# Kernel tuning notes

Hardware: AMD Instinct MI355X
Metric: run time of the kernel (lower is better)

Reference implementation:

```python
import jax, jax.numpy as jnp
import numpy as np

GRID = 16
K = 2
NW = (GRID - K + 1) ** 2  # 225 sliding 2x2 windows on the 16x16 grid


def _make_mask():
    idx = np.arange(GRID * GRID).reshape(GRID, GRID)
    wins = np.stack([idx[i:i + K, j:j + K].ravel()
                     for i in range(GRID - K + 1) for j in range(GRID - K + 1)])
    m = np.zeros((NW, GRID * GRID), np.float32)
    m[np.arange(NW)[:, None], wins] = 1.0
    return jnp.asarray(m)

MASK = _make_mask()          # [225, 256] window -> covered cells
MASK_COUNT = MASK.sum(0)     # windows covering each cell
BN_SCALE = np.float32(1.0 / np.sqrt(1.0 + 1e-5))  # eval BN, running mean=0 var=1


def _adapter(x, w1, w2):
    return jax.nn.relu(jax.nn.relu(x @ w1.T) @ w2.T)


def _bn(x, g, b):
    return x * (g * BN_SCALE) + b


def _head(x, w1, b1, g2, be2, w2, b2, g3, be3, w3, b3):
    x = _bn(jax.nn.relu(x @ w1.T + b1), g2, be2)
    x = _bn(jax.nn.relu(x @ w2.T + b2), g3, be3)
    return jax.nn.sigmoid(x @ w3.T + b3)[:, 0]


def setup_inputs() -> dict:
    B, L, P, D, R, S = 64, 3, 225, 640, 1800, 240
    key = jax.random.key(0)
    ks = jax.random.split(key, 16)
    n = lambda k, s, sc=1.0: jax.random.normal(k, s, jnp.float32) * sc
    te = n(ks[3], (2, D)); te = te / jnp.linalg.norm(te, axis=-1, keepdims=True)
    pr = n(ks[5], (L, R, D)); pr = pr / jnp.linalg.norm(pr, axis=-1, keepdims=True)
    w = 0.05
    return dict(
        image=n(ks[0], (B, 3, S, S)),
        image_embeds=n(ks[1], (B, D)),
        patch_embeds=n(ks[2], (L, B, P, D)),
        text_embeds=te,
        image_embeds_ref=n(ks[4], (1, D)),
        patch_embeds_ref=pr,
        a_w1=n(ks[6], (160, D), w), a_w2=n(ks[7], (D, 160), w),
        r_w1=n(ks[8], (128, D), w), r_b1=jnp.zeros((128,)),
        r_g2=jnp.ones((128,)), r_be2=jnp.zeros((128,)),
        r_w2=n(ks[9], (64, 128), w), r_b2=jnp.zeros((64,)),
        r_g3=jnp.ones((64,)), r_be3=jnp.zeros((64,)),
        r_w3=n(ks[10], (1, 64), w), r_b3=jnp.zeros((1,)),
        h_w1=n(ks[11], (128, P), w), h_b1=jnp.zeros((128,)),
        h_g2=jnp.ones((128,)), h_be2=jnp.zeros((128,)),
        h_w2=n(ks[12], (64, 128), w), h_b2=jnp.zeros((64,)),
        h_g3=jnp.ones((64,)), h_be3=jnp.zeros((64,)),
        h_w3=n(ks[13], (1, 64), w), h_b3=jnp.zeros((1,)),
    )


def reference(image, image_embeds, patch_embeds, text_embeds, image_embeds_ref,
              patch_embeds_ref, a_w1, a_w2,
              r_w1, r_b1, r_g2, r_be2, r_w2, r_b2, r_g3, r_be3, r_w3, r_b3,
              h_w1, h_b1, h_g2, h_be2, h_w2, h_b2, h_g3, h_be3, h_w3, h_b3):
    pe = patch_embeds / jnp.linalg.norm(patch_embeds, axis=-1, keepdims=True)
    nie = image_embeds / jnp.linalg.norm(image_embeds, axis=-1, keepdims=True)
    text_score = jax.nn.softmax(100.0 * nie @ text_embeds.T, axis=-1)[:, 1]
    # kNN-style min-distance over reference patches: [L,B,P,R]
    sim = jnp.einsum('lbpd,lrd->lbpr', pe, patch_embeds_ref)
    patch_ref_map = ((1.0 - sim).min(axis=3) / 2.0).mean(axis=0)  # [B,P]
    fg_score = patch_ref_map.max(axis=1)
    diff = image_embeds_ref - _adapter(image_embeds, a_w1, a_w2)
    img_ref_score = _head(diff, r_w1, r_b1, r_g2, r_be2, r_w2, r_b2, r_g3, r_be3, r_w3, r_b3)
    holistic = (text_score + img_ref_score)[:, None] + patch_ref_map  # [B,225]
    hl_score = _head(holistic, h_w1, h_b1, h_g2, h_be2, h_w2, h_b2, h_g3, h_be3, h_w3, h_b3)
    final_score = (hl_score + fg_score) / 2.0
    # harmonic aggregation of window scores onto the 16x16 grid
    heat = (MASK_COUNT / ((1.0 / holistic) @ MASK)).reshape(-1, GRID, GRID)
    hmap = jax.image.resize(heat, (heat.shape[0], image.shape[2], image.shape[3]), 'bilinear')
    return final_score, hmap
```

## Files before the change

### kernel.cpp

```cpp
#include <hip/hip_runtime.h>
#include <stdint.h>
#include <math.h>

#define L_DIM 3
#define B_DIM 64
#define P_DIM 225
#define D_DIM 640
#define R_DIM 1800
#define S_DIM 240
#define M_TOT 14400
#define M_PAD 14592
#define N_PAD 2048
#define MT 57
#define NT 8
#define KT 10
#define BNSCALE 0.99999500003749981f

typedef __bf16 bf16x8 __attribute__((ext_vector_type(8)));
typedef float f32x4 __attribute__((ext_vector_type(4)));

__device__ __forceinline__ unsigned short f2bf(float f) {
    union { float f; unsigned u; } v; v.f = f;
    unsigned u = v.u;
    unsigned r = (u + 0x7FFFu + ((u >> 16) & 1u)) >> 16;
    return (unsigned short)r;
}

__global__ __launch_bounds__(256)
void k_convert(const float* __restrict__ pe, const float* __restrict__ per,
               unsigned short* __restrict__ abf, unsigned short* __restrict__ rbf,
               float* __restrict__ rnorm)
{
    const int AROWS = L_DIM * M_PAD;
    int wid = (blockIdx.x * 256 + threadIdx.x) >> 6;
    int lane = threadIdx.x & 63;
    const ushort4 z4 = {0, 0, 0, 0};
    if (wid < AROWS) {
        int l = wid / M_PAD, r = wid - l * M_PAD;
        unsigned short* dst = abf + (size_t)wid * D_DIM;
        if (r < M_TOT) {
            const float4* src = (const float4*)(pe + ((size_t)l * M_TOT + r) * D_DIM);
            float ss = 0.f;
            #pragma unroll
            for (int it = 0; it < 3; ++it) {
                int idx = it * 64 + lane;
                if (idx < 160) {
                    float4 v = src[idx];
                    ss += v.x * v.x + v.y * v.y + v.z * v.z + v.w * v.w;
                    ushort4 o;
                    o.x = f2bf(v.x); o.y = f2bf(v.y); o.z = f2bf(v.z); o.w = f2bf(v.w);
                    *(ushort4*)(dst + idx * 4) = o;
                }
            }
            #pragma unroll
            for (int m = 32; m; m >>= 1) ss += __shfl_xor(ss, m);
            if (lane == 0) rnorm[l * M_TOT + r] = rsqrtf(ss);
        } else {
            #pragma unroll
            for (int it = 0; it < 3; ++it) {
                int idx = it * 64 + lane;
                if (idx < 160) *(ushort4*)(dst + idx * 4) = z4;
            }
        }
    } else {
        int w2 = wid - AROWS;
        int l = w2 / N_PAD, r = w2 - l * N_PAD;
        unsigned short* dst = rbf + (size_t)w2 * D_DIM;
        if (r < R_DIM) {
            const float4* src = (const float4*)(per + ((size_t)l * R_DIM + r) * D_DIM);
            #pragma unroll
            for (int it = 0; it < 3; ++it) {
                int idx = it * 64 + lane;
                if (idx < 160) {
                    float4 v = src[idx];
                    ushort4 o;
                    o.x = f2bf(v.x); o.y = f2bf(v.y); o.z = f2bf(v.z); o.w = f2bf(v.w);
                    *(ushort4*)(dst + idx * 4) = o;
                }
            }
        } else {
            #pragma unroll
            for (int it = 0; it < 3; ++it) {
                int idx = it * 64 + lane;
                if (idx < 160) *(ushort4*)(dst + idx * 4) = z4;
            }
        }
    }
}

#define MFMA(A, B, C) __builtin_amdgcn_mfma_f32_16x16x32_bf16((A), (B), (C), 0, 0, 0)
#define GLL(SRC, DSTOFF)                                                     \
    __builtin_amdgcn_global_load_lds(                                        \
        (const __attribute__((address_space(1))) void*)(SRC),               \
        (__attribute__((address_space(3))) void*)(lds + (DSTOFF)), 16, 0, 0)

#define PHASE_TAIL(NJB, STG0, STG1, VMSTR)                                   \
    {                                                                        \
        bf16x8 b00 = *(const bf16x8*)(lds + bB + (brow0 + (NJB) * 16) * 64 + sw0);     \
        bf16x8 b01 = *(const bf16x8*)(lds + bB + (brow0 + (NJB) * 16) * 64 + sw1);     \
        bf16x8 b10 = *(const bf16x8*)(lds + bB + (brow0 + (NJB + 1) * 16) * 64 + sw0); \
        bf16x8 b11 = *(const bf16x8*)(lds + bB + (brow0 + (NJB + 1) * 16) * 64 + sw1); \
        STG0; STG1;                                                          \
        asm volatile("s_waitcnt " VMSTR ::: "memory");                       \
        __builtin_amdgcn_s_barrier();                                        \
        __builtin_amdgcn_s_setprio(1);                                       \
        _Pragma("unroll")                                                    \
        for (int mi = 0; mi < 4; ++mi) {                                     \
            acc[mi][NJB]     = MFMA(a[mi][0], b00, acc[mi][NJB]);            \
            acc[mi][NJB]     = MFMA(a[mi][1], b01, acc[mi][NJB]);            \
            acc[mi][NJB + 1] = MFMA(a[mi][0], b10, acc[mi][NJB + 1]);        \
            acc[mi][NJB + 1] = MFMA(a[mi][1], b11, acc[mi][NJB + 1]);        \
        }                                                                    \
        __builtin_amdgcn_s_setprio(0);                                       \
    }

__global__ __launch_bounds__(512, 2)
void k_gemm_max(const unsigned short* __restrict__ abf,
                const unsigned short* __restrict__ rbf,
                float* __restrict__ pmax)
{
    __shared__ unsigned short lds[65536];
    __shared__ float red[2][256];

    int bid = blockIdx.x;
    int v = (bid & 7) * 171 + (bid >> 3);
    int l = v / (MT * NT);
    int rem = v - l * (MT * NT);
    int mt = rem >> 3;
    int nt = rem & 7;

    int tid = threadIdx.x;
    int wid = tid >> 6, lane = tid & 63;
    int wm = wid >> 1;
    int wn = wid & 1;
    int lane15 = lane & 15, lg = lane >> 4;
    int sA = lane15 & 7;
    int sw0 = ((lg) ^ sA) << 3;
    int sw1 = ((4 + lg) ^ sA) << 3;
    int arow0 = wm * 64 + lane15;
    int brow0 = wn * 128 + lane15;

    int rowc = lane >> 3;
    int scol = ((lane & 7) ^ rowc) << 3;
    const unsigned short* gA = abf + (size_t)(l * M_PAD + mt * 256) * D_DIM;
    const unsigned short* gB = rbf + (size_t)(l * N_PAD + nt * 256) * D_DIM;
    int chA0 = wid, chA1 = 8 + wid, chA2 = 16 + wid, chA3 = 24 + wid;
    int chB0 = (wid < 4) ? (0 + wid) : (12 + wid);
    int chB1 = (wid < 4) ? (4 + wid) : (16 + wid);
    int chB2 = (wid < 4) ? (8 + wid) : (20 + wid);
    int chB3 = (wid < 4) ? (12 + wid) : (24 + wid);
    const unsigned short* pA0 = gA + (size_t)(chA0 * 8 + rowc) * D_DIM + scol;
    const unsigned short* pA1 = gA + (size_t)(chA1 * 8 + rowc) * D_DIM + scol;
    const unsigned short* pA2 = gA + (size_t)(chA2 * 8 + rowc) * D_DIM + scol;
    const unsigned short* pA3 = gA + (size_t)(chA3 * 8 + rowc) * D_DIM + scol;
    const unsigned short* pB0 = gB + (size_t)(chB0 * 8 + rowc) * D_DIM + scol;
    const unsigned short* pB1 = gB + (size_t)(chB1 * 8 + rowc) * D_DIM + scol;
    const unsigned short* pB2 = gB + (size_t)(chB2 * 8 + rowc) * D_DIM + scol;
    const unsigned short* pB3 = gB + (size_t)(chB3 * 8 + rowc) * D_DIM + scol;

    f32x4 acc[4][8];
    #pragma unroll
    for (int mi = 0; mi < 4; ++mi)
        #pragma unroll
        for (int nj = 0; nj < 8; ++nj)
            acc[mi][nj] = f32x4{0.f, 0.f, 0.f, 0.f};

    GLL(pA0, chA0 * 512); GLL(pA1, chA1 * 512);
    GLL(pA2, chA2 * 512); GLL(pA3, chA3 * 512);
    GLL(pB0, 32768 + chB0 * 512); GLL(pB1, 32768 + chB1 * 512);
    GLL(pB2, 32768 + chB2 * 512); GLL(pB3, 32768 + chB3 * 512);
    asm volatile("s_waitcnt vmcnt(3)" ::: "memory");
    __builtin_amdgcn_s_barrier();

    int buf = 0;
    for (int kt = 0; kt < KT; ++kt) {
        int ob = buf ^ 1;
        int aB = buf * 16384;
        int bB = 32768 + buf * 16384;
        int oaB = ob * 16384;
        int obB = 32768 + ob * 16384;
        int koff = (kt + 1 < KT ? kt + 1 : KT - 1) * 64;

        bf16x8 a[4][2];
        #pragma unroll
        for (int mi = 0; mi < 4; ++mi) {
            a[mi][0] = *(const bf16x8*)(lds + aB + (arow0 + mi * 16) * 64 + sw0);
            a[mi][1] = *(const bf16x8*)(lds + aB + (arow0 + mi * 16) * 64 + sw1);
        }
        PHASE_TAIL(0, GLL(pA0 + koff, oaB + chA0 * 512),
                      GLL(pA1 + koff, oaB + chA1 * 512), "vmcnt(4)")
        PHASE_TAIL(2, GLL(pA2 + koff, oaB + chA2 * 512),
                      GLL(pA3 + koff, oaB + chA3 * 512), "vmcnt(5)")
        PHASE_TAIL(4, GLL(pB0 + koff, obB + chB0 * 512),
                      GLL(pB1 + koff, obB + chB1 * 512), "vmcnt(6)")
        PHASE_TAIL(6, GLL(pB2 + koff, obB + chB2 * 512),
                      GLL(pB3 + koff, obB + chB3 * 512), "vmcnt(3)")
        buf = ob;
    }

    __syncthreads();

    int colbase = nt * 256 + wn * 128 + lane15;
    #pragma unroll
    for (int mi = 0; mi < 4; ++mi) {
        float t[4] = {-__builtin_inff(), -__builtin_inff(),
                      -__builtin_inff(), -__builtin_inff()};
        #pragma unroll
        for (int nj = 0; nj < 8; ++nj) {
            if (colbase + nj * 16 < R_DIM) {
                #pragma unroll
                for (int r = 0; r < 4; ++r) t[r] = fmaxf(t[r], acc[mi][nj][r]);
            }
        }
        #pragma unroll
        for (int m = 1; m <= 8; m <<= 1) {
            #pragma unroll
            for (int r = 0; r < 4; ++r) t[r] = fmaxf(t[r], __shfl_xor(t[r], m));
        }
        if (lane15 == 0) {
            int rb = wm * 64 + mi * 16 + lg * 4;
            #pragma unroll
            for (int r = 0; r < 4; ++r) red[wn][rb + r] = t[r];
        }
    }
    __syncthreads();
    if (tid < 256) {
        float vmx = fmaxf(red[0][tid], red[1][tid]);
        pmax[((size_t)l * NT + nt) * M_PAD + mt * 256 + tid] = vmx;
    }
}

__device__ __forceinline__ float block_sum8(float v, volatile float* scratch) {
    #pragma unroll
    for (int m = 32; m; m >>= 1) v += __shfl_xor(v, m);
    int w = threadIdx.x >> 6;
    __syncthreads();
    if ((threadIdx.x & 63) == 0) scratch[w] = v;
    __syncthreads();
    float r = 0.f;
    #pragma unroll
    for (int i = 0; i < 8; ++i) r += scratch[i];
    return r;
}
__device__ __forceinline__ float block_max8(float v, volatile float* scratch) {
    #pragma unroll
    for (int m = 32; m; m >>= 1) v = fmaxf(v, __shfl_xor(v, m));
    int w = threadIdx.x >> 6;
    __syncthreads();
    if ((threadIdx.x & 63) == 0) scratch[w] = v;
    __syncthreads();
    float r = scratch[0];
    #pragma unroll
    for (int i = 1; i < 8; ++i) r = fmaxf(r, scratch[i]);
    return r;
}

__global__ __launch_bounds__(512)
void k_small(const float* __restrict__ ie, const float* __restrict__ te,
             const float* __restrict__ ier,
             const float* __restrict__ a_w1, const float* __restrict__ a_w2,
             const float* __restrict__ r_w1, const float* __restrict__ r_b1,
             const float* __restrict__ r_g2, const float* __restrict__ r_be2,
             const float* __restrict__ r_w2, const float* __restrict__ r_b2,
             const float* __restrict__ r_g3, const float* __restrict__ r_be3,
             const float* __restrict__ r_w3, const float* __restrict__ r_b3,
             const float* __restrict__ h_w1, const float* __restrict__ h_b1,
             const float* __restrict__ h_g2, const float* __restrict__ h_be2,
             const float* __restrict__ h_w2, const float* __restrict__ h_b2,
             const float* __restrict__ h_g3, const float* __restrict__ h_be3,
             const float* __restrict__ h_w3, const float* __restrict__ h_b3,
             const float* __restrict__ pmax, const float* __restrict__ rnorm,
             float* __restrict__ heat, float* __restrict__ out_score)
{
    int b = blockIdx.x, tid = threadIdx.x;
    __shared__ float x[D_DIM];
    __shared__ float h1[160];
    __shared__ float dif[D_DIM];
    __shared__ float z1[128];
    __shared__ float z2[64];
    __shared__ float hol[P_DIM];
    __shared__ float rcp[P_DIM];
    __shared__ float scratch[8];

    for (int i = tid; i < D_DIM; i += 512) x[i] = ie[b * D_DIM + i];
    __syncthreads();

    float ss = 0.f, d0 = 0.f, d1 = 0.f;
    for (int i = tid; i < D_DIM; i += 512) {
        float v = x[i];
        ss += v * v;
        d0 += v * te[i];
        d1 += v * te[D_DIM + i];
    }
    float ssum = block_sum8(ss, scratch);
    float dd0 = block_sum8(d0, scratch);
    float dd1 = block_sum8(d1, scratch);
    float tscore = 1.f / (1.f + expf(100.f * rsqrtf(ssum) * (dd0 - dd1)));

    for (int o = tid; o < 160; o += 512) {
        const float* w = a_w1 + (size_t)o * D_DIM;
        float s0 = 0, s1 = 0, s2 = 0, s3 = 0;
        for (int d = 0; d < D_DIM; d += 4) {
            s0 += x[d] * w[d]; s1 += x[d + 1] * w[d + 1];
            s2 += x[d + 2] * w[d + 2]; s3 += x[d + 3] * w[d + 3];
        }
        h1[o] = fmaxf((s0 + s1) + (s2 + s3), 0.f);
    }
    __syncthreads();
    for (int d = tid; d < D_DIM; d += 512) {
        const float* w = a_w2 + (size_t)d * 160;
        float s0 = 0, s1 = 0, s2 = 0, s3 = 0;
        for (int o = 0; o < 160; o += 4) {
            s0 += h1[o] * w[o]; s1 += h1[o + 1] * w[o + 1];
            s2 += h1[o + 2] * w[o + 2]; s3 += h1[o + 3] * w[o + 3];
        }
        dif[d] = ier[d] - fmaxf((s0 + s1) + (s2 + s3), 0.f);
    }
    __syncthreads();

    for (int o = tid; o < 128; o += 512) {
        const float* w = r_w1 + (size_t)o * D_DIM;
        float s0 = 0, s1 = 0, s2 = 0, s3 = 0;
        for (int d = 0; d < D_DIM; d += 4) {
            s0 += dif[d] * w[d]; s1 += dif[d + 1] * w[d + 1];
            s2 += dif[d + 2] * w[d + 2]; s3 += dif[d + 3] * w[d + 3];
        }
        float s = (s0 + s1) + (s2 + s3) + r_b1[o];
        z1[o] = fmaxf(s, 0.f) * (r_g2[o] * BNSCALE) + r_be2[o];
    }
    __syncthreads();
    for (int o = tid; o < 64; o += 512) {
        const float* w = r_w2 + (size_t)o * 128;
        float s = r_b2[o];
        for (int d = 0; d < 128; ++d) s += z1[d] * w[d];
        z2[o] = fmaxf(s, 0.f) * (r_g3[o] * BNSCALE) + r_be3[o];
    }
    __syncthreads();
    float sp = (tid < 64) ? z2[tid] * r_w3[tid] : 0.f;
    float irs = 1.f / (1.f + expf(-(block_sum8(sp, scratch) + r_b3[0])));

    float fgp = -__builtin_inff();
    float base = tscore + irs;
    for (int p = tid; p < P_DIM; p += 512) {
        int r = b * P_DIM + p;
        float s = 0.f;
        #pragma unroll
        for (int l = 0; l < L_DIM; ++l) {
            float m = -__builtin_inff();
            #pragma unroll
            for (int t = 0; t < NT; ++t)
                m = fmaxf(m, pmax[((size_t)l * NT + t) * M_PAD + r]);
            s += m * rnorm[l * M_TOT + r];
        }
        float pv = (3.0f - s) / 6.0f;
        fgp = fmaxf(fgp, pv);
        float h = base + pv;
        hol[p] = h;
        rcp[p] = 1.f / h;
    }
    float fg = block_max8(fgp, scratch);

    for (int o = tid; o < 128; o += 512) {
        const float* w = h_w1 + (size_t)o * P_DIM;
        float s = h_b1[o];
        for (int d = 0; d < P_DIM; ++d) s += hol[d] * w[d];
        z1[o] = fmaxf(s, 0.f) * (h_g2[o] * BNSCALE) + h_be2[o];
    }
    __syncthreads();
    for (int o = tid; o < 64; o += 512) {
        const float* w = h_w2 + (size_t)o * 128;
        float s = h_b2[o];
        for (int d = 0; d < 128; ++d) s += z1[d] * w[d];
        z2[o] = fmaxf(s, 0.f) * (h_g3[o] * BNSCALE) + h_be3[o];
    }
    __syncthreads();
    float sp2 = (tid < 64) ? z2[tid] * h_w3[tid] : 0.f;
    float hl_in = block_sum8(sp2, scratch) + h_b3[0];
    if (tid == 0) {
        float hl = 1.f / (1.f + expf(-hl_in));
        out_score[b] = (hl + fg) * 0.5f;
    }

    if (tid < 256) {
        int r = tid >> 4, c = tid & 15;
        float s = 0.f, cnt = 0.f;
        #pragma unroll
        for (int di = -1; di <= 0; ++di) {
            int i = r + di;
            if (i < 0 || i > 14) continue;
            #pragma unroll
            for (int dj = -1; dj <= 0; ++dj) {
                int j = c + dj;
                if (j < 0 || j > 14) continue;
                s += rcp[i * 15 + j];
                cnt += 1.f;
            }
        }
        heat[b * 256 + tid] = cnt / s;
    }
}

__global__ __launch_bounds__(256)
void k_resize(const float* __restrict__ heat, float* __restrict__ outh)
{
    int b = blockIdx.x >> 3, sub = blockIdx.x & 7;
    __shared__ float h[256];
    if (threadIdx.x < 256) h[threadIdx.x] = heat[b * 256 + threadIdx.x];
    __syncthreads();
    int base = sub * 30 * S_DIM;
    for (int q = threadIdx.x; q < 30 * S_DIM; q += 256) {
        int px = base + q;
        int y = px / S_DIM, xc = px - y * S_DIM;
        float sy = fminf(fmaxf((y - 7) * (1.0f / 15.0f), 0.f), 15.f);
        float sx = fminf(fmaxf((xc - 7) * (1.0f / 15.0f), 0.f), 15.f);
        int y0 = (int)sy, x0 = (int)sx;
        int y1 = min(y0 + 1, 15), x1 = min(x0 + 1, 15);
        float fy = sy - (float)y0, fx = sx - (float)x0;
        float v00 = h[y0 * 16 + x0], v01 = h[y0 * 16 + x1];
        float v10 = h[y1 * 16 + x0], v11 = h[y1 * 16 + x1];
        float v = (1.f - fy) * ((1.f - fx) * v00 + fx * v01)
                + fy * ((1.f - fx) * v10 + fx * v11);
        outh[(size_t)b * (S_DIM * S_DIM) + px] = v;
    }
}

extern "C" void kernel_launch(void* const* d_in, const int* in_sizes, int n_in,
                              void* d_out, int out_size, void* d_ws, size_t ws_size,
                              hipStream_t stream)
{
    (void)in_sizes; (void)n_in; (void)out_size; (void)ws_size;
    const float* image_embeds = (const float*)d_in[1];
    const float* patch_embeds = (const float*)d_in[2];
    const float* text_embeds  = (const float*)d_in[3];
    const float* ier          = (const float*)d_in[4];
    const float* per          = (const float*)d_in[5];
    const float* a_w1 = (const float*)d_in[6];
    const float* a_w2 = (const float*)d_in[7];
    const float* r_w1 = (const float*)d_in[8];
    const float* r_b1 = (const float*)d_in[9];
    const float* r_g2 = (const float*)d_in[10];
    const float* r_be2 = (const float*)d_in[11];
    const float* r_w2 = (const float*)d_in[12];
    const float* r_b2 = (const float*)d_in[13];
    const float* r_g3 = (const float*)d_in[14];
    const float* r_be3 = (const float*)d_in[15];
    const float* r_w3 = (const float*)d_in[16];
    const float* r_b3 = (const float*)d_in[17];
    const float* h_w1 = (const float*)d_in[18];
    const float* h_b1 = (const float*)d_in[19];
    const float* h_g2 = (const float*)d_in[20];
    const float* h_be2 = (const float*)d_in[21];
    const float* h_w2 = (const float*)d_in[22];
    const float* h_b2 = (const float*)d_in[23];
    const float* h_g3 = (const float*)d_in[24];
    const float* h_be3 = (const float*)d_in[25];
    const float* h_w3 = (const float*)d_in[26];
    const float* h_b3 = (const float*)d_in[27];

    char* ws = (char*)d_ws;
    size_t off = 0;
    auto take = [&](size_t bytes) -> void* {
        void* p = ws + off;
        off += (bytes + 255) & ~(size_t)255;
        return p;
    };
    float* rnorm = (float*)take((size_t)L_DIM * M_TOT * 4);
    float* pmax  = (float*)take((size_t)L_DIM * NT * M_PAD * 4);
    float* heat  = (float*)take((size_t)B_DIM * 256 * 4);
    unsigned short* abf = (unsigned short*)take((size_t)L_DIM * M_PAD * D_DIM * 2);
    unsigned short* rbf = (unsigned short*)take((size_t)L_DIM * N_PAD * D_DIM * 2);

    float* out_f = (float*)d_out;

    k_convert<<<dim3((L_DIM * M_PAD + L_DIM * N_PAD) / 4), dim3(256), 0, stream>>>(
        patch_embeds, per, abf, rbf, rnorm);
    k_gemm_max<<<dim3(L_DIM * MT * NT), dim3(512), 0, stream>>>(abf, rbf, pmax);
    k_small<<<dim3(B_DIM), dim3(512), 0, stream>>>(image_embeds, text_embeds, ier,
        a_w1, a_w2, r_w1, r_b1, r_g2, r_be2, r_w2, r_b2, r_g3, r_be3, r_w3, r_b3,
        h_w1, h_b1, h_g2, h_be2, h_w2, h_b2, h_g3, h_be3, h_w3, h_b3,
        pmax, rnorm, heat, out_f);
    k_resize<<<dim3(B_DIM * 8), dim3(256), 0, stream>>>(heat, out_f + B_DIM);
}
```

Measured before the change: 202.9 us.

## Switch GEMM-max kernel to 32x32x16 MFMA tiles

Replaces the 16x16x32 bf16 MFMA instructions in the similarity GEMM with 32x32x16 ones. The per-wave fragment layout, LDS swizzled reads, accumulator shapes and max-reduction epilogue are all reworked to match. The goal is fewer LDS fragment reads per FLOP and higher MFMA throughput per instruction. It also lowers launch_bounds occupancy from 2 blocks to 1, which frees registers but may reduce latency hiding.

```diff
diff --git a/kernel.cpp b/kernel.cpp
--- a/kernel.cpp
+++ b/kernel.cpp
@@ -17,7 +17,7 @@
 #define BNSCALE 0.99999500003749981f
 
 typedef __bf16 bf16x8 __attribute__((ext_vector_type(8)));
-typedef float f32x4 __attribute__((ext_vector_type(4)));
+typedef float f32x16 __attribute__((ext_vector_type(16)));
 
 __device__ __forceinline__ unsigned short f2bf(float f) {
     union { float f; unsigned u; } v; v.f = f;
@@ -88,33 +88,34 @@
     }
 }
 
-#define MFMA(A, B, C) __builtin_amdgcn_mfma_f32_16x16x32_bf16((A), (B), (C), 0, 0, 0)
+#define MFMA32(A, B, C) __builtin_amdgcn_mfma_f32_32x32x16_bf16((A), (B), (C), 0, 0, 0)
 #define GLL(SRC, DSTOFF)                                                     \
     __builtin_amdgcn_global_load_lds(                                        \
         (const __attribute__((address_space(1))) void*)(SRC),               \
         (__attribute__((address_space(3))) void*)(lds + (DSTOFF)), 16, 0, 0)
 
-#define PHASE_TAIL(NJB, STG0, STG1, VMSTR)                                   \
+#define PHASE32(P, STG0, STG1, VMSTR)                                        \
     {                                                                        \
-        bf16x8 b00 = *(const bf16x8*)(lds + bB + (brow0 + (NJB) * 16) * 64 + sw0);     \
-        bf16x8 b01 = *(const bf16x8*)(lds + bB + (brow0 + (NJB) * 16) * 64 + sw1);     \
-        bf16x8 b10 = *(const bf16x8*)(lds + bB + (brow0 + (NJB + 1) * 16) * 64 + sw0); \
-        bf16x8 b11 = *(const bf16x8*)(lds + bB + (brow0 + (NJB + 1) * 16) * 64 + sw1); \
+        bf16x8 b0 = *(const bf16x8*)(lds + bB + (bcol + (P) * 32) * 64 + kc0); \
+        bf16x8 b1 = *(const bf16x8*)(lds + bB + (bcol + (P) * 32) * 64 + kc1); \
+        bf16x8 b2 = *(const bf16x8*)(lds + bB + (bcol + (P) * 32) * 64 + kc2); \
+        bf16x8 b3 = *(const bf16x8*)(lds + bB + (bcol + (P) * 32) * 64 + kc3); \
         STG0; STG1;                                                          \
         asm volatile("s_waitcnt " VMSTR ::: "memory");                       \
         __builtin_amdgcn_s_barrier();                                        \
         __builtin_amdgcn_s_setprio(1);                                       \
-        _Pragma("unroll")                                                    \
-        for (int mi = 0; mi < 4; ++mi) {                                     \
-            acc[mi][NJB]     = MFMA(a[mi][0], b00, acc[mi][NJB]);            \
-            acc[mi][NJB]     = MFMA(a[mi][1], b01, acc[mi][NJB]);            \
-            acc[mi][NJB + 1] = MFMA(a[mi][0], b10, acc[mi][NJB + 1]);        \
-            acc[mi][NJB + 1] = MFMA(a[mi][1], b11, acc[mi][NJB + 1]);        \
-        }                                                                    \
+        acc[0][P] = MFMA32(a[0][0], b0, acc[0][P]);                          \
+        acc[1][P] = MFMA32(a[1][0], b0, acc[1][P]);                          \
+        acc[0][P] = MFMA32(a[0][1], b1, acc[0][P]);                          \
+        acc[1][P] = MFMA32(a[1][1], b1, acc[1][P]);                          \
+        acc[0][P] = MFMA32(a[0][2], b2, acc[0][P]);                          \
+        acc[1][P] = MFMA32(a[1][2], b2, acc[1][P]);                          \
+        acc[0][P] = MFMA32(a[0][3], b3, acc[0][P]);                          \
+        acc[1][P] = MFMA32(a[1][3], b3, acc[1][P]);                          \
         __builtin_amdgcn_s_setprio(0);                                       \
     }
 
-__global__ __launch_bounds__(512, 2)
+__global__ __launch_bounds__(512, 1)
 void k_gemm_max(const unsigned short* __restrict__ abf,
                 const unsigned short* __restrict__ rbf,
                 float* __restrict__ pmax)
@@ -133,12 +134,14 @@
     int wid = tid >> 6, lane = tid & 63;
     int wm = wid >> 1;
     int wn = wid & 1;
-    int lane15 = lane & 15, lg = lane >> 4;
-    int sA = lane15 & 7;
-    int sw0 = ((lg) ^ sA) << 3;
-    int sw1 = ((4 + lg) ^ sA) << 3;
-    int arow0 = wm * 64 + lane15;
-    int brow0 = wn * 128 + lane15;
+    int lane31 = lane & 31, lhi = lane >> 5;
+    int s7 = lane31 & 7;
+    int kc0 = ((0 + lhi) ^ s7) << 3;
+    int kc1 = ((2 + lhi) ^ s7) << 3;
+    int kc2 = ((4 + lhi) ^ s7) << 3;
+    int kc3 = ((6 + lhi) ^ s7) << 3;
+    int arow = wm * 64 + lane31;
+    int bcol = wn * 128 + lane31;
 
     int rowc = lane >> 3;
     int scol = ((lane & 7) ^ rowc) << 3;
@@ -158,12 +161,14 @@
     const unsigned short* pB2 = gB + (size_t)(chB2 * 8 + rowc) * D_DIM + scol;
     const unsigned short* pB3 = gB + (size_t)(chB3 * 8 + rowc) * D_DIM + scol;
 
-    f32x4 acc[4][8];
-    #pragma unroll
-    for (int mi = 0; mi < 4; ++mi)
-        #pragma unroll
-        for (int nj = 0; nj < 8; ++nj)
-            acc[mi][nj] = f32x4{0.f, 0.f, 0.f, 0.f};
+    f32x16 acc[2][4];
+    #pragma unroll
+    for (int mi = 0; mi < 2; ++mi)
+        #pragma unroll
+        for (int nj = 0; nj < 4; ++nj)
+            #pragma unroll
+            for (int e = 0; e < 16; ++e)
+                acc[mi][nj][e] = 0.f;
 
     GLL(pA0, chA0 * 512); GLL(pA1, chA1 * 512);
     GLL(pA2, chA2 * 512); GLL(pA3, chA3 * 512);
@@ -181,46 +186,50 @@
         int obB = 32768 + ob * 16384;
         int koff = (kt + 1 < KT ? kt + 1 : KT - 1) * 64;
 
-        bf16x8 a[4][2];
-        #pragma unroll
-        for (int mi = 0; mi < 4; ++mi) {
-            a[mi][0] = *(const bf16x8*)(lds + aB + (arow0 + mi * 16) * 64 + sw0);
-            a[mi][1] = *(const bf16x8*)(lds + aB + (arow0 + mi * 16) * 64 + sw1);
-        }
-        PHASE_TAIL(0, GLL(pA0 + koff, oaB + chA0 * 512),
-                      GLL(pA1 + koff, oaB + chA1 * 512), "vmcnt(4)")
-        PHASE_TAIL(2, GLL(pA2 + koff, oaB + chA2 * 512),
-                      GLL(pA3 + koff, oaB + chA3 * 512), "vmcnt(5)")
-        PHASE_TAIL(4, GLL(pB0 + koff, obB + chB0 * 512),
-                      GLL(pB1 + koff, obB + chB1 * 512), "vmcnt(6)")
-        PHASE_TAIL(6, GLL(pB2 + koff, obB + chB2 * 512),
-                      GLL(pB3 + koff, obB + chB3 * 512), "vmcnt(3)")
+        bf16x8 a[2][4];
+        #pragma unroll
+        for (int mi = 0; mi < 2; ++mi) {
+            a[mi][0] = *(const bf16x8*)(lds + aB + (arow + mi * 32) * 64 + kc0);
+            a[mi][1] = *(const bf16x8*)(lds + aB + (arow + mi * 32) * 64 + kc1);
+            a[mi][2] = *(const bf16x8*)(lds + aB + (arow + mi * 32) * 64 + kc2);
+            a[mi][3] = *(const bf16x8*)(lds + aB + (arow + mi * 32) * 64 + kc3);
+        }
+        PHASE32(0, GLL(pA0 + koff, oaB + chA0 * 512),
+                   GLL(pA1 + koff, oaB + chA1 * 512), "vmcnt(4)")
+        PHASE32(1, GLL(pA2 + koff, oaB + chA2 * 512),
+                   GLL(pA3 + koff, oaB + chA3 * 512), "vmcnt(5)")
+        PHASE32(2, GLL(pB0 + koff, obB + chB0 * 512),
+                   GLL(pB1 + koff, obB + chB1 * 512), "vmcnt(6)")
+        PHASE32(3, GLL(pB2 + koff, obB + chB2 * 512),
+                   GLL(pB3 + koff, obB + chB3 * 512), "vmcnt(3)")
         buf = ob;
     }
 
     __syncthreads();
 
-    int colbase = nt * 256 + wn * 128 + lane15;
-    #pragma unroll
-    for (int mi = 0; mi < 4; ++mi) {
-        float t[4] = {-__builtin_inff(), -__builtin_inff(),
-                      -__builtin_inff(), -__builtin_inff()};
-        #pragma unroll
-        for (int nj = 0; nj < 8; ++nj) {
-            if (colbase + nj * 16 < R_DIM) {
+    int colbase = nt * 256 + wn * 128 + lane31;
+    #pragma unroll
+    for (int mi = 0; mi < 2; ++mi) {
+        float t[16];
+        #pragma unroll
+        for (int r = 0; r < 16; ++r) t[r] = -__builtin_inff();
+        #pragma unroll
+        for (int nj = 0; nj < 4; ++nj) {
+            if (colbase + nj * 32 < R_DIM) {
                 #pragma unroll
-                for (int r = 0; r < 4; ++r) t[r] = fmaxf(t[r], acc[mi][nj][r]);
-            }
-        }
-        #pragma unroll
-        for (int m = 1; m <= 8; m <<= 1) {
-            #pragma unroll
-            for (int r = 0; r < 4; ++r) t[r] = fmaxf(t[r], __shfl_xor(t[r], m));
-        }
-        if (lane15 == 0) {
-            int rb = wm * 64 + mi * 16 + lg * 4;
-            #pragma unroll
-            for (int r = 0; r < 4; ++r) red[wn][rb + r] = t[r];
+                for (int r = 0; r < 16; ++r) t[r] = fmaxf(t[r], acc[mi][nj][r]);
+            }
+        }
+        #pragma unroll
+        for (int m = 1; m <= 16; m <<= 1) {
+            #pragma unroll
+            for (int r = 0; r < 16; ++r) t[r] = fmaxf(t[r], __shfl_xor(t[r], m));
+        }
+        if (lane31 == 0) {
+            int rb = wm * 64 + mi * 32 + lhi * 4;
+            #pragma unroll
+            for (int r = 0; r < 16; ++r)
+                red[wn][rb + (r & 3) + 8 * (r >> 2)] = t[r];
         }
     }
     __syncthreads();
```

Measured after the change: 229.6 us. 1.13x slower.

## Split reference padding: GEMM over 1792 columns plus small remainder kernel

Applied to the files above, without the earlier changes.

The reference dimension was padded from 1800 to 2048, so a full eighth 256-column tile was mostly padding. The main GEMM now covers 1792 columns in 7 tiles, and a new small MFMA kernel handles the last 8 reference rows, writing a per-row max that seeds the reduction in k_small. The XCD block remapping is rebalanced for the 1197-block grid. This trades about an eighth less GEMM work for an extra kernel launch and an extra buffer.

```diff
diff --git a/kernel.cpp b/kernel.cpp
--- a/kernel.cpp
+++ b/kernel.cpp
@@ -10,9 +10,9 @@
 #define S_DIM 240
 #define M_TOT 14400
 #define M_PAD 14592
-#define N_PAD 2048
+#define N_PAD 1792
 #define MT 57
-#define NT 8
+#define NT 7
 #define KT 10
 #define BNSCALE 0.99999500003749981f
 
@@ -29,9 +29,10 @@
 __global__ __launch_bounds__(256)
 void k_convert(const float* __restrict__ pe, const float* __restrict__ per,
                unsigned short* __restrict__ abf, unsigned short* __restrict__ rbf,
-               float* __restrict__ rnorm)
+               unsigned short* __restrict__ rbf8, float* __restrict__ rnorm)
 {
     const int AROWS = L_DIM * M_PAD;
+    const int BROWS = L_DIM * N_PAD;
     int wid = (blockIdx.x * 256 + threadIdx.x) >> 6;
     int lane = threadIdx.x & 63;
     const ushort4 z4 = {0, 0, 0, 0};
@@ -62,12 +63,27 @@
                 if (idx < 160) *(ushort4*)(dst + idx * 4) = z4;
             }
         }
-    } else {
+    } else if (wid < AROWS + BROWS) {
         int w2 = wid - AROWS;
         int l = w2 / N_PAD, r = w2 - l * N_PAD;
         unsigned short* dst = rbf + (size_t)w2 * D_DIM;
-        if (r < R_DIM) {
-            const float4* src = (const float4*)(per + ((size_t)l * R_DIM + r) * D_DIM);
+        const float4* src = (const float4*)(per + ((size_t)l * R_DIM + r) * D_DIM);
+        #pragma unroll
+        for (int it = 0; it < 3; ++it) {
+            int idx = it * 64 + lane;
+            if (idx < 160) {
+                float4 v = src[idx];
+                ushort4 o;
+                o.x = f2bf(v.x); o.y = f2bf(v.y); o.z = f2bf(v.z); o.w = f2bf(v.w);
+                *(ushort4*)(dst + idx * 4) = o;
+            }
+        }
+    } else {
+        int w3 = wid - AROWS - BROWS;
+        int l = w3 >> 4, r = w3 & 15;
+        unsigned short* dst = rbf8 + (size_t)(l * 16 + r) * D_DIM;
+        if (r < 8) {
+            const float4* src = (const float4*)(per + ((size_t)l * R_DIM + 1792 + r) * D_DIM);
             #pragma unroll
             for (int it = 0; it < 3; ++it) {
                 int idx = it * 64 + lane;
@@ -123,11 +139,12 @@
     __shared__ float red[2][256];
 
     int bid = blockIdx.x;
-    int v = (bid & 7) * 171 + (bid >> 3);
+    int xcd = bid & 7, idx = bid >> 3;
+    int v = (xcd < 5 ? xcd * 150 : 750 + (xcd - 5) * 149) + idx;
     int l = v / (MT * NT);
     int rem = v - l * (MT * NT);
-    int mt = rem >> 3;
-    int nt = rem & 7;
+    int mt = rem / NT;
+    int nt = rem - mt * NT;
 
     int tid = threadIdx.x;
     int wid = tid >> 6, lane = tid & 63;
@@ -200,17 +217,14 @@
 
     __syncthreads();
 
-    int colbase = nt * 256 + wn * 128 + lane15;
     #pragma unroll
     for (int mi = 0; mi < 4; ++mi) {
         float t[4] = {-__builtin_inff(), -__builtin_inff(),
                       -__builtin_inff(), -__builtin_inff()};
         #pragma unroll
         for (int nj = 0; nj < 8; ++nj) {
-            if (colbase + nj * 16 < R_DIM) {
-                #pragma unroll
-                for (int r = 0; r < 4; ++r) t[r] = fmaxf(t[r], acc[mi][nj][r]);
-            }
+            #pragma unroll
+            for (int r = 0; r < 4; ++r) t[r] = fmaxf(t[r], acc[mi][nj][r]);
         }
         #pragma unroll
         for (int m = 1; m <= 8; m <<= 1) {
@@ -227,6 +241,55 @@
     if (tid < 256) {
         float vmx = fmaxf(red[0][tid], red[1][tid]);
         pmax[((size_t)l * NT + nt) * M_PAD + mt * 256 + tid] = vmx;
+    }
+}
+
+__global__ __launch_bounds__(256)
+void k_rem(const unsigned short* __restrict__ abf,
+           const unsigned short* __restrict__ rbf8,
+           float* __restrict__ rmax8)
+{
+    __shared__ unsigned short ldsb[16 * D_DIM];
+    int bid = blockIdx.x;
+    int rflat0 = bid * 64;
+    int l = rflat0 / M_TOT;
+    int tid = threadIdx.x;
+
+    {
+        const unsigned* src = (const unsigned*)(rbf8 + (size_t)l * 16 * D_DIM);
+        unsigned* dst = (unsigned*)ldsb;
+        #pragma unroll
+        for (int i = 0; i < 20; ++i) dst[i * 256 + tid] = src[i * 256 + tid];
+    }
+    __syncthreads();
+
+    int w = tid >> 6, lane = tid & 63;
+    int lane15 = lane & 15, lg = lane >> 4;
+    int rl = (rflat0 - l * M_TOT) + w * 16;
+
+    const unsigned short* arow = abf + (size_t)(l * M_PAD + rl + lane15) * D_DIM;
+    const unsigned short* brow = ldsb + (size_t)lane15 * D_DIM;
+
+    f32x4 acc = f32x4{0.f, 0.f, 0.f, 0.f};
+    for (int kk = 0; kk < D_DIM; kk += 32) {
+        bf16x8 a = *(const bf16x8*)(arow + kk + lg * 8);
+        bf16x8 b = *(const bf16x8*)(brow + kk + lg * 8);
+        acc = MFMA(a, b, acc);
+    }
+
+    float t[4];
+    #pragma unroll
+    for (int r = 0; r < 4; ++r)
+        t[r] = (lane15 < 8) ? acc[r] : -__builtin_inff();
+    #pragma unroll
+    for (int m = 1; m <= 8; m <<= 1) {
+        #pragma unroll
+        for (int r = 0; r < 4; ++r) t[r] = fmaxf(t[r], __shfl_xor(t[r], m));
+    }
+    if (lane15 == 0) {
+        #pragma unroll
+        for (int r = 0; r < 4; ++r)
+            rmax8[(size_t)l * M_TOT + rl + lg * 4 + r] = t[r];
     }
 }
 
@@ -269,7 +332,8 @@
              const float* __restrict__ h_w2, const float* __restrict__ h_b2,
              const float* __restrict__ h_g3, const float* __restrict__ h_be3,
              const float* __restrict__ h_w3, const float* __restrict__ h_b3,
-             const float* __restrict__ pmax, const float* __restrict__ rnorm,
+             const float* __restrict__ pmax, const float* __restrict__ rmax8,
+             const float* __restrict__ rnorm,
              float* __restrict__ heat, float* __restrict__ out_score)
 {
     int b = blockIdx.x, tid = threadIdx.x;
@@ -346,7 +410,7 @@
         float s = 0.f;
         #pragma unroll
         for (int l = 0; l < L_DIM; ++l) {
-            float m = -__builtin_inff();
+            float m = rmax8[(size_t)l * M_TOT + r];
             #pragma unroll
             for (int t = 0; t < NT; ++t)
                 m = fmaxf(m, pmax[((size_t)l * NT + t) * M_PAD + r]);
@@ -466,18 +530,21 @@
     };
     float* rnorm = (float*)take((size_t)L_DIM * M_TOT * 4);
     float* pmax  = (float*)take((size_t)L_DIM * NT * M_PAD * 4);
+    float* rmax8 = (float*)take((size_t)L_DIM * M_TOT * 4);
     float* heat  = (float*)take((size_t)B_DIM * 256 * 4);
-    unsigned short* abf = (unsigned short*)take((size_t)L_DIM * M_PAD * D_DIM * 2);
-    unsigned short* rbf = (unsigned short*)take((size_t)L_DIM * N_PAD * D_DIM * 2);
+    unsigned short* abf  = (unsigned short*)take((size_t)L_DIM * M_PAD * D_DIM * 2);
+    unsigned short* rbf  = (unsigned short*)take((size_t)L_DIM * N_PAD * D_DIM * 2);
+    unsigned short* rbf8 = (unsigned short*)take((size_t)L_DIM * 16 * D_DIM * 2);
 
     float* out_f = (float*)d_out;
 
-    k_convert<<<dim3((L_DIM * M_PAD + L_DIM * N_PAD) / 4), dim3(256), 0, stream>>>(
-        patch_embeds, per, abf, rbf, rnorm);
+    k_convert<<<dim3((L_DIM * M_PAD + L_DIM * N_PAD + L_DIM * 16) / 4), dim3(256), 0, stream>>>(
+        patch_embeds, per, abf, rbf, rbf8, rnorm);
     k_gemm_max<<<dim3(L_DIM * MT * NT), dim3(512), 0, stream>>>(abf, rbf, pmax);
+    k_rem<<<dim3(L_DIM * M_TOT / 64), dim3(256), 0, stream>>>(abf, rbf8, rmax8);
     k_small<<<dim3(B_DIM), dim3(512), 0, stream>>>(image_embeds, text_embeds, ier,
         a_w1, a_w2, r_w1, r_b1, r_g2, r_be2, r_w2, r_b2, r_g3, r_be3, r_w3, r_b3,
         h_w1, h_b1, h_g2, h_be2, h_w2, h_b2, h_g3, h_be3, h_w3, h_b3,
-        pmax, rnorm, heat, out_f);
+        pmax, rmax8, rnorm, heat, out_f);
     k_resize<<<dim3(B_DIM * 8), dim3(256), 0, stream>>>(heat, out_f + B_DIM);
 }
```

Result: faster. 192.7 us (-5.0%).
